# Performance work log

Hardware: AMD Instinct MI355X
Metric: run time of the kernel (lower is better)

Reference implementation:

```python
import jax, jax.numpy as jnp
import numpy as np

N = 100000        # nodes (== node_num)
E = 3200000       # edges
C = 8             # hidden (sparse=False branch)
HEADS = 2
GROUPS = 8
LAYERS = 3
FEAT = 16
EMB = 8
NCLS = 2


def glin(x, W, b):
    # PyG grouped Linear: x [..., C], W [G, C//G, C//G], b [C]
    G, cin, cout = W.shape
    xg = x.reshape(*x.shape[:-1], G, cin)
    out = jnp.einsum('...gi,gio->...go', xg, W)
    return out.reshape(*x.shape[:-1], G * cout) + b


def gcn_norm(edge_index, num_nodes):
    # symmetric GCN normalization with added self-loops, unit edge weights
    loop = jnp.arange(num_nodes, dtype=edge_index.dtype)
    src = jnp.concatenate([edge_index[0], loop])
    dst = jnp.concatenate([edge_index[1], loop])
    w = jnp.ones(src.shape[0], dtype=jnp.float32)
    deg = jax.ops.segment_sum(w, dst, num_segments=num_nodes)
    dinv = jnp.where(deg > 0, jax.lax.rsqrt(deg), 0.0)
    return src, dst, dinv[src] * dinv[dst]


def dna_conv(x_all, src, dst, norm, Wq, bq, Wk, bk, Wv, bv):
    # PyG DNAConv (eval mode): target's latest history entry attends over the
    # source neighbor's full history. x_all: [N, L, C].
    n, L, c = x_all.shape
    d = c // HEADS
    # q/k/v linears are per-entry -> compute per node, gather per edge (same math)
    q = glin(x_all[:, -1], Wq, bq).reshape(n, HEADS, d)    # [N,H,d]
    k = glin(x_all, Wk, bk).reshape(n, L, HEADS, d)        # [N,L,H,d]
    v = glin(x_all, Wv, bv).reshape(n, L, HEADS, d)
    qe = q[dst]                                            # [E',H,d]
    score = jnp.einsum('ehd,elhd->ehl', qe, k[src]) * (1.0 / np.sqrt(d))
    attn = jax.nn.softmax(score, axis=-1)                  # softmax over history L
    out = jnp.einsum('ehl,elhd->ehd', attn, v[src]).reshape(-1, c)
    out = out * norm[:, None]
    return jax.ops.segment_sum(out, dst, num_segments=n)   # aggr='add' at target


def setup_inputs():
    ks = jax.random.split(jax.random.key(0), 16)
    s = 0.5
    return {
        'x': jax.random.normal(ks[0], (N, FEAT), dtype=jnp.float32),
        'node_index': jnp.arange(N),
        'node_one_hot': jnp.zeros((N,), dtype=jnp.int32),
        'edge_index': jax.random.randint(ks[1], (2, E), 0, N),
        'edge_weight': jax.random.uniform(ks[2], (E,), dtype=jnp.float32),
        'emb_table': jax.random.normal(ks[3], (N, EMB), dtype=jnp.float32) * 0.1,
        'W1': jax.random.normal(ks[4], (EMB + FEAT, C), dtype=jnp.float32) * 0.2,
        'b1': jnp.zeros((C,), dtype=jnp.float32),
        'Wq': jax.random.normal(ks[5], (LAYERS, GROUPS, C // GROUPS, C // GROUPS), dtype=jnp.float32) * s,
        'bq': jnp.zeros((LAYERS, C), dtype=jnp.float32),
        'Wk': jax.random.normal(ks[6], (LAYERS, GROUPS, C // GROUPS, C // GROUPS), dtype=jnp.float32) * s,
        'bk': jnp.zeros((LAYERS, C), dtype=jnp.float32),
        'Wv': jax.random.normal(ks[7], (LAYERS, GROUPS, C // GROUPS, C // GROUPS), dtype=jnp.float32) * s,
        'bv': jnp.zeros((LAYERS, C), dtype=jnp.float32),
        'W2': jax.random.normal(ks[8], (C, NCLS), dtype=jnp.float32) * 0.3,
        'b2': jnp.zeros((NCLS,), dtype=jnp.float32),
    }


def reference(x, node_index, node_one_hot, edge_index, edge_weight,
              emb_table, W1, b1, Wq, bq, Wk, bk, Wv, bv, W2, b2):
    # node_one_hot / edge_weight are unpacked but unused in the original forward
    h = jnp.concatenate([emb_table[node_index], x], axis=1)   # [N, EMB+FEAT]
    h = jax.nn.relu(h @ W1 + b1)                              # [N, C]
    x_all = h[:, None, :]                                     # history [N, 1, C]
    src, dst, norm = gcn_norm(edge_index, x.shape[0])
    for i in range(LAYERS):
        h = jax.nn.relu(dna_conv(x_all, src, dst, norm,
                                 Wq[i], bq[i], Wk[i], bk[i], Wv[i], bv[i]))
        x_all = jnp.concatenate([x_all, h[:, None, :]], axis=1)
    logits = x_all[:, -1] @ W2 + b2
    return jax.nn.log_softmax(logits, axis=-1)
```

## Files before the change

kernel.cpp:

```cpp
#include <hip/hip_runtime.h>
#include <math.h>


#define SBB   8
#define SBN   256
#define CH    4096
#define CAP   9216

typedef _Float16 half8 __attribute__((ext_vector_type(8)));
typedef int int4v __attribute__((ext_vector_type(4)));

__global__ void __launch_bounds__(256) phaseAC(const int* __restrict__ eidx,
                                               int* __restrict__ gcnt,
                                               int* __restrict__ ebuf,
                                               int E, int NS) {
    __shared__ int sorted_[CH];
    __shared__ unsigned short karr[CH];
    __shared__ int cntS[512];
    __shared__ int lofs[512];
    __shared__ int wbase[512];
    __shared__ int sA[512], sB[512];
    int t = threadIdx.x, b = blockIdx.x;
    int base = b * CH;
    int nEdge = E - base; if (nEdge > CH) nEdge = CH;

    for (int i = t; i < 512; i += 256) cntS[i] = 0;
    __syncthreads();

    int w[16]; short kk[16];
#pragma unroll
    for (int it = 0; it < 4; it++) {
        int e0 = base + (it * 256 + t) * 4;
        if (e0 + 3 < E) {
            int4v s4 = __builtin_nontemporal_load((const int4v*)(eidx + e0));
            int4v d4 = __builtin_nontemporal_load((const int4v*)(eidx + E + e0));
#pragma unroll
            for (int j = 0; j < 4; j++) {
                int idx = it * 4 + j;
                w[idx] = s4[j] | ((d4[j] & (SBN - 1)) << 17);
                kk[idx] = (short)(d4[j] >> SBB);
                atomicAdd(&cntS[kk[idx]], 1);
            }
        } else {
#pragma unroll
            for (int j = 0; j < 4; j++) {
                int e = e0 + j, idx = it * 4 + j;
                if (e < E) {
                    int s = eidx[e], d = eidx[E + e];
                    w[idx] = s | ((d & (SBN - 1)) << 17);
                    kk[idx] = (short)(d >> SBB);
                    atomicAdd(&cntS[kk[idx]], 1);
                } else { w[idx] = 0; kk[idx] = 511; }
            }
        }
    }
    __syncthreads();
    sA[t] = cntS[t]; sA[t + 256] = cntS[t + 256];
    __syncthreads();
    int* sp = sA; int* dp = sB;
    for (int o = 1; o < 512; o <<= 1) {
#pragma unroll
        for (int h = 0; h < 2; h++) {
            int i = t + h * 256;
            int v = sp[i];
            if (i >= o) v += sp[i - o];
            dp[i] = v;
        }
        __syncthreads();
        int* tmp = sp; sp = dp; dp = tmp;
    }
    for (int i = t; i < 512; i += 256) {
        int excl = sp[i] - cntS[i];
        lofs[i] = excl;
        if (i < NS && cntS[i] > 0) {
            int g = atomicAdd(&gcnt[i], cntS[i]);
            wbase[i] = i * CAP + g - excl;
        }
    }
    __syncthreads();
#pragma unroll
    for (int idx = 0; idx < 16; idx++) {
        if (kk[idx] != 511) {
            int p = atomicAdd(&lofs[kk[idx]], 1);
            sorted_[p] = w[idx];
            karr[p] = (unsigned short)kk[idx];
        }
    }
    __syncthreads();
    for (int i = t; i < nEdge; i += 256)
        ebuf[wbase[karr[i]] + i] = sorted_[i];
}

__global__ void super_csr(int* __restrict__ ebuf, const int* __restrict__ gcnt,
                          unsigned int* __restrict__ off, char* __restrict__ A,
                          char* __restrict__ U, int NS, int n) {
    __shared__ int seg[CAP];
    __shared__ int cnt[SBN];
    __shared__ int fillp[SBN];
    __shared__ int sd[256];
    int t = threadIdx.x, k = blockIdx.x;
    cnt[t] = 0;
    int start = k * CAP;
    int len = gcnt[k];
    __syncthreads();
    for (int i = t; i < len; i += 256) {
        int w = __builtin_nontemporal_load(&ebuf[start + i]);
        seg[i] = w;
        atomicAdd(&cnt[w >> 17], 1);
    }
    __syncthreads();
    int v = cnt[t];
    sd[t] = v; __syncthreads();
    for (int o = 1; o < 256; o <<= 1) {
        int u = 0; if (t >= o) u = sd[t - o];
        __syncthreads(); sd[t] += u; __syncthreads();
    }
    int excl = sd[t] - v;
    fillp[t] = excl;
    int d = (k << SBB) + t;
    if (d < n) {
        off[d] = (unsigned int)(start + excl) | ((unsigned int)v << 22);
        float dvv = rsqrtf((float)(v + 1));
        *(float*)(A + (size_t)d * 32 + 16) = dvv;
        *(float*)(U + (size_t)d * 64 + 48) = dvv;
    }
    __syncthreads();
    for (int i = t; i < len; i += 256) {
        int w = seg[i];
        int pos = atomicAdd(&fillp[w >> 17], 1);
        ebuf[start + pos] = w & 131071;
    }
}

__global__ void node_init(const float* __restrict__ x, const int* __restrict__ nidx,
                          const float* __restrict__ emb, const float* __restrict__ W1,
                          const float* __restrict__ b1, char* __restrict__ A,
                          char* __restrict__ U, int n) {
    int i = blockIdx.x * blockDim.x + threadIdx.x;
    if (i >= n) return;
    float in[24];
    int ni = nidx[i];
    const float4* ep = (const float4*)(emb + (size_t)ni * 8);
    float4 e0 = ep[0], e1 = ep[1];
    in[0] = e0.x; in[1] = e0.y; in[2] = e0.z; in[3] = e0.w;
    in[4] = e1.x; in[5] = e1.y; in[6] = e1.z; in[7] = e1.w;
    const float4* xp = (const float4*)(x + (size_t)i * 16);
#pragma unroll
    for (int t = 0; t < 4; t++) {
        float4 v = xp[t];
        in[8 + 4 * t + 0] = v.x; in[8 + 4 * t + 1] = v.y;
        in[8 + 4 * t + 2] = v.z; in[8 + 4 * t + 3] = v.w;
    }
    float acc[8];
#pragma unroll
    for (int j = 0; j < 8; j++) acc[j] = b1[j];
#pragma unroll
    for (int t = 0; t < 24; t++) {
        float xv = in[t];
#pragma unroll
        for (int j = 0; j < 8; j++) acc[j] = fmaf(xv, W1[t * 8 + j], acc[j]);
    }
    half8 h;
#pragma unroll
    for (int j = 0; j < 8; j++) h[j] = (_Float16)fmaxf(acc[j], 0.0f);
    *(half8*)(A + (size_t)i * 32) = h;
    *(half8*)(U + (size_t)i * 64) = h;
}

template <int Li>
__device__ __forceinline__ void attn_out(const float* xs, const float* qv,
                                         const float* __restrict__ wk, const float* __restrict__ bk,
                                         const float* __restrict__ wv, const float* __restrict__ bv,
                                         float* out) {
    float score[2][Li];
#pragma unroll
    for (int l = 0; l < Li; l++) {
#pragma unroll
        for (int h = 0; h < 2; h++) {
            float sc = 0.f;
#pragma unroll
            for (int dd = 0; dd < 4; dd++) {
                int c = h * 4 + dd;
                sc = fmaf(qv[c], fmaf(xs[l * 8 + c], wk[c], bk[c]), sc);
            }
            score[h][l] = 0.5f * sc;
        }
    }
    float attn[2][Li];
#pragma unroll
    for (int h = 0; h < 2; h++) {
        float m = score[h][0];
#pragma unroll
        for (int l = 1; l < Li; l++) m = fmaxf(m, score[h][l]);
        float ssum = 0.f;
#pragma unroll
        for (int l = 0; l < Li; l++) { attn[h][l] = __expf(score[h][l] - m); ssum += attn[h][l]; }
        float inv = 1.0f / ssum;
#pragma unroll
        for (int l = 0; l < Li; l++) attn[h][l] *= inv;
    }
#pragma unroll
    for (int c = 0; c < 8; c++) {
        int h = c >> 2;
        float o = 0.f;
#pragma unroll
        for (int l = 0; l < Li; l++) o = fmaf(attn[h][l], fmaf(xs[l * 8 + c], wv[c], bv[c]), o);
        out[c] = o;
    }
}

template <int Li, bool LAST>
__global__ void agg_layer(const int* __restrict__ ssrc, const unsigned int* __restrict__ off,
                          const char* __restrict__ A, char* __restrict__ U,
                          const float* __restrict__ wq, const float* __restrict__ bq,
                          const float* __restrict__ wk, const float* __restrict__ bk,
                          const float* __restrict__ wv, const float* __restrict__ bv,
                          const float* __restrict__ W2, const float* __restrict__ b2,
                          float* __restrict__ out, int n) {
    int tid = blockIdx.x * blockDim.x + threadIdx.x;
    int d = tid >> 3, t = tid & 7;
    if (d >= n) return;
    unsigned int ow = off[d];
    int lo = (int)(ow & 0x3FFFFFu), cnt = (int)(ow >> 22);

    half8 qh;
    if (Li == 1) qh = *(const half8*)(A + (size_t)d * 32);
    else if (Li == 2) qh = *(const half8*)(U + (size_t)d * 64 + 16);
    else qh = *(const half8*)(U + (size_t)d * 64 + 32);
    float qv[8];
#pragma unroll
    for (int c = 0; c < 8; c++) qv[c] = fmaf((float)qh[c], wq[c], bq[c]);

    float acc[8];
#pragma unroll
    for (int c = 0; c < 8; c++) acc[c] = 0.f;

    int total = cnt + 1;
    int g = (total + 7) >> 3;
    int j0 = t * g;
    int j1 = j0 + g; if (j1 > total) j1 = total;

    for (int j = j0; j < j1; j += 4) {
        int m = j1 - j; if (m > 4) m = 4;
        int sidx[4];
#pragma unroll
        for (int u = 0; u < 4; u++) {
            int idx = j + u;
            sidx[u] = (u < m) ? ((idx == 0) ? d : ssrc[lo + idx - 1]) : d;
        }
        half8 r[4][Li]; float nsv[4];
#pragma unroll
        for (int u = 0; u < 4; u++) {
            if (u < m) {
                if (Li == 1) {
                    const char* p = A + (size_t)sidx[u] * 32;
                    r[u][0] = *(const half8*)p;
                    nsv[u] = *(const float*)(p + 16);
                } else {
                    const char* p = U + (size_t)sidx[u] * 64;
#pragma unroll
                    for (int l = 0; l < Li; l++) r[u][l] = *(const half8*)(p + l * 16);
                    nsv[u] = *(const float*)(p + 48);
                }
            }
        }
#pragma unroll
        for (int u = 0; u < 4; u++) {
            if (u < m) {
                float xs[8 * Li];
#pragma unroll
                for (int l = 0; l < Li; l++)
#pragma unroll
                    for (int c = 0; c < 8; c++) xs[l * 8 + c] = (float)r[u][l][c];
                float o[8];
                attn_out<Li>(xs, qv, wk, bk, wv, bv, o);
#pragma unroll
                for (int c = 0; c < 8; c++) acc[c] = fmaf(o[c], nsv[u], acc[c]);
            }
        }
    }
#pragma unroll
    for (int m2 = 1; m2 < 8; m2 <<= 1) {
#pragma unroll
        for (int c = 0; c < 8; c++) acc[c] += __shfl_xor(acc[c], m2);
    }
    float nd = (Li == 1) ? *(const float*)(A + (size_t)d * 32 + 16)
                         : *(const float*)(U + (size_t)d * 64 + 48);
    if (!LAST) {
        float h = fmaxf(acc[t] * nd, 0.f);
        *(_Float16*)(U + (size_t)d * 64 + Li * 16 + 2 * t) = (_Float16)h;
    } else if (t == 0) {
        float z0 = b2[0], z1 = b2[1];
#pragma unroll
        for (int c = 0; c < 8; c++) {
            float h = fmaxf(acc[c] * nd, 0.f);
            z0 = fmaf(h, W2[c * 2 + 0], z0);
            z1 = fmaf(h, W2[c * 2 + 1], z1);
        }
        float m2 = fmaxf(z0, z1);
        float lse = m2 + logf(__expf(z0 - m2) + __expf(z1 - m2));
        ((float2*)out)[d] = make_float2(z0 - lse, z1 - lse);
    }
}

extern "C" void kernel_launch(void* const* d_in, const int* in_sizes, int n_in,
                              void* d_out, int out_size, void* d_ws, size_t ws_size,
                              hipStream_t stream) {
    const float* x    = (const float*)d_in[0];
    const int*   nidx = (const int*)d_in[1];
    const int*   eidx = (const int*)d_in[3];
    const float* emb  = (const float*)d_in[5];
    const float* W1   = (const float*)d_in[6];
    const float* b1   = (const float*)d_in[7];
    const float* Wq   = (const float*)d_in[8];
    const float* bq   = (const float*)d_in[9];
    const float* Wk   = (const float*)d_in[10];
    const float* bk   = (const float*)d_in[11];
    const float* Wv   = (const float*)d_in[12];
    const float* bv   = (const float*)d_in[13];
    const float* W2   = (const float*)d_in[14];
    const float* b2   = (const float*)d_in[15];
    float* out = (float*)d_out;

    const int n = in_sizes[0] / 16;
    const int E = in_sizes[3] / 2;
    const int NS = (n + SBN - 1) / SBN;
    const int NBLK = (E + CH - 1) / CH;

    char* wsp = (char*)d_ws;
    char*  A     = wsp;                      wsp += (size_t)n * 32;
    char*  U     = wsp;                      wsp += (size_t)n * 64;
    int*   ebuf  = (int*)wsp;                wsp += (size_t)NS * CAP * 4;
    unsigned int* off = (unsigned int*)wsp;  wsp += (size_t)n * 4;
    int*   gcnt  = (int*)wsp;                wsp += (size_t)NS * 4;

    dim3 blk(256);
    dim3 gn((n + 255) / 256);
    dim3 ga(((size_t)n * 8 + 255) / 256);

    (void)hipMemsetAsync(gcnt, 0, (size_t)NS * 4, stream);
    phaseAC<<<NBLK, blk, 0, stream>>>(eidx, gcnt, ebuf, E, NS);
    super_csr<<<NS, blk, 0, stream>>>(ebuf, gcnt, off, A, U, NS, n);
    node_init<<<gn, blk, 0, stream>>>(x, nidx, emb, W1, b1, A, U, n);

    agg_layer<1, false><<<ga, blk, 0, stream>>>(ebuf, off, A, U,
        Wq, bq, Wk, bk, Wv, bv, W2, b2, out, n);
    agg_layer<2, false><<<ga, blk, 0, stream>>>(ebuf, off, A, U,
        Wq + 8, bq + 8, Wk + 8, bk + 8, Wv + 8, bv + 8, W2, b2, out, n);
    agg_layer<3, true><<<ga, blk, 0, stream>>>(ebuf, off, A, U,
        Wq + 16, bq + 16, Wk + 16, bk + 16, Wv + 16, bv + 16, W2, b2, out, n);
}
```

Baseline: 276.8 us.

## Factor V linear out of edge loop and skip softmax for single history

Uses linearity to pull the diagonal value projection (wv, bv) out of the per-edge sum: edges now accumulate a norm-weighted attention mix of the raw history plus the sum of norms, and wv/bv are applied once per node. The key scale and the 1/sqrt(d) factor are folded into the query once per node. With a single history entry the softmax is identically one, so layer 1 reduces to a plain weighted sum, and its gather batch grows from 4 to 8. This cuts per-edge arithmetic, relying on the grouped weights being diagonal (C/G = 1) and on bk being constant across history entries so it cancels in the softmax.

```diff
diff --git a/kernel.cpp b/kernel.cpp
--- a/kernel.cpp
+++ b/kernel.cpp
@@ -167,48 +167,6 @@
     *(half8*)(U + (size_t)i * 64) = h;
 }
 
-template <int Li>
-__device__ __forceinline__ void attn_out(const float* xs, const float* qv,
-                                         const float* __restrict__ wk, const float* __restrict__ bk,
-                                         const float* __restrict__ wv, const float* __restrict__ bv,
-                                         float* out) {
-    float score[2][Li];
-#pragma unroll
-    for (int l = 0; l < Li; l++) {
-#pragma unroll
-        for (int h = 0; h < 2; h++) {
-            float sc = 0.f;
-#pragma unroll
-            for (int dd = 0; dd < 4; dd++) {
-                int c = h * 4 + dd;
-                sc = fmaf(qv[c], fmaf(xs[l * 8 + c], wk[c], bk[c]), sc);
-            }
-            score[h][l] = 0.5f * sc;
-        }
-    }
-    float attn[2][Li];
-#pragma unroll
-    for (int h = 0; h < 2; h++) {
-        float m = score[h][0];
-#pragma unroll
-        for (int l = 1; l < Li; l++) m = fmaxf(m, score[h][l]);
-        float ssum = 0.f;
-#pragma unroll
-        for (int l = 0; l < Li; l++) { attn[h][l] = __expf(score[h][l] - m); ssum += attn[h][l]; }
-        float inv = 1.0f / ssum;
-#pragma unroll
-        for (int l = 0; l < Li; l++) attn[h][l] *= inv;
-    }
-#pragma unroll
-    for (int c = 0; c < 8; c++) {
-        int h = c >> 2;
-        float o = 0.f;
-#pragma unroll
-        for (int l = 0; l < Li; l++) o = fmaf(attn[h][l], fmaf(xs[l * 8 + c], wv[c], bv[c]), o);
-        out[c] = o;
-    }
-}
-
 template <int Li, bool LAST>
 __global__ void agg_layer(const int* __restrict__ ssrc, const unsigned int* __restrict__ off,
                           const char* __restrict__ A, char* __restrict__ U,
@@ -217,40 +175,44 @@
                           const float* __restrict__ wv, const float* __restrict__ bv,
                           const float* __restrict__ W2, const float* __restrict__ b2,
                           float* __restrict__ out, int n) {
+    constexpr int B = (Li == 1) ? 8 : 4;
     int tid = blockIdx.x * blockDim.x + threadIdx.x;
     int d = tid >> 3, t = tid & 7;
     if (d >= n) return;
     unsigned int ow = off[d];
     int lo = (int)(ow & 0x3FFFFFu), cnt = (int)(ow >> 22);
 
-    half8 qh;
-    if (Li == 1) qh = *(const half8*)(A + (size_t)d * 32);
-    else if (Li == 2) qh = *(const half8*)(U + (size_t)d * 64 + 16);
-    else qh = *(const half8*)(U + (size_t)d * 64 + 32);
-    float qv[8];
-#pragma unroll
-    for (int c = 0; c < 8; c++) qv[c] = fmaf((float)qh[c], wq[c], bq[c]);
-
-    float acc[8];
-#pragma unroll
-    for (int c = 0; c < 8; c++) acc[c] = 0.f;
+    float qk[8];
+    if (Li >= 2) {
+        half8 qh = (Li == 2) ? *(const half8*)(U + (size_t)d * 64 + 16)
+                             : *(const half8*)(U + (size_t)d * 64 + 32);
+#pragma unroll
+        for (int c = 0; c < 8; c++) {
+            float qv = fmaf((float)qh[c], wq[c], bq[c]);
+            qk[c] = 0.5f * wk[c] * qv;
+        }
+    }
+
+    float T[8]; float SN = 0.f;
+#pragma unroll
+    for (int c = 0; c < 8; c++) T[c] = 0.f;
 
     int total = cnt + 1;
     int g = (total + 7) >> 3;
     int j0 = t * g;
     int j1 = j0 + g; if (j1 > total) j1 = total;
 
-    for (int j = j0; j < j1; j += 4) {
-        int m = j1 - j; if (m > 4) m = 4;
-        int sidx[4];
-#pragma unroll
-        for (int u = 0; u < 4; u++) {
+    for (int j = j0; j < j1; j += B) {
+        int m = j1 - j; if (m > B) m = B;
+        int sidx[B];
+#pragma unroll
+        for (int u = 0; u < B; u++) {
             int idx = j + u;
             sidx[u] = (u < m) ? ((idx == 0) ? d : ssrc[lo + idx - 1]) : d;
         }
-        half8 r[4][Li]; float nsv[4];
-#pragma unroll
-        for (int u = 0; u < 4; u++) {
+        half8 r[B][Li]; float nsv[B];
+#pragma unroll
+        for (int u = 0; u < B; u++) {
             if (u < m) {
                 if (Li == 1) {
                     const char* p = A + (size_t)sidx[u] * 32;
@@ -265,35 +227,75 @@
             }
         }
 #pragma unroll
-        for (int u = 0; u < 4; u++) {
+        for (int u = 0; u < B; u++) {
             if (u < m) {
                 float xs[8 * Li];
 #pragma unroll
                 for (int l = 0; l < Li; l++)
 #pragma unroll
                     for (int c = 0; c < 8; c++) xs[l * 8 + c] = (float)r[u][l][c];
-                float o[8];
-                attn_out<Li>(xs, qv, wk, bk, wv, bv, o);
-#pragma unroll
-                for (int c = 0; c < 8; c++) acc[c] = fmaf(o[c], nsv[u], acc[c]);
+                float ns = nsv[u];
+                if (Li == 1) {
+#pragma unroll
+                    for (int c = 0; c < 8; c++) T[c] = fmaf(ns, xs[c], T[c]);
+                    SN += ns;
+                } else {
+                    float score[2][Li];
+#pragma unroll
+                    for (int l = 0; l < Li; l++) {
+#pragma unroll
+                        for (int h = 0; h < 2; h++) {
+                            float sc = 0.f;
+#pragma unroll
+                            for (int dd = 0; dd < 4; dd++) {
+                                int c = h * 4 + dd;
+                                sc = fmaf(qk[c], xs[l * 8 + c], sc);
+                            }
+                            score[h][l] = sc;
+                        }
+                    }
+                    float e[2][Li], nsh[2];
+#pragma unroll
+                    for (int h = 0; h < 2; h++) {
+                        float mx = score[h][0];
+#pragma unroll
+                        for (int l = 1; l < Li; l++) mx = fmaxf(mx, score[h][l]);
+                        float ssum = 0.f;
+#pragma unroll
+                        for (int l = 0; l < Li; l++) { e[h][l] = __expf(score[h][l] - mx); ssum += e[h][l]; }
+                        nsh[h] = ns / ssum;
+                    }
+#pragma unroll
+                    for (int c = 0; c < 8; c++) {
+                        int h = c >> 2;
+                        float P = 0.f;
+#pragma unroll
+                        for (int l = 0; l < Li; l++) P = fmaf(e[h][l], xs[l * 8 + c], P);
+                        T[c] = fmaf(nsh[h], P, T[c]);
+                    }
+                    SN += ns;
+                }
             }
         }
     }
 #pragma unroll
     for (int m2 = 1; m2 < 8; m2 <<= 1) {
 #pragma unroll
-        for (int c = 0; c < 8; c++) acc[c] += __shfl_xor(acc[c], m2);
+        for (int c = 0; c < 8; c++) T[c] += __shfl_xor(T[c], m2);
+        SN += __shfl_xor(SN, m2);
     }
     float nd = (Li == 1) ? *(const float*)(A + (size_t)d * 32 + 16)
                          : *(const float*)(U + (size_t)d * 64 + 48);
     if (!LAST) {
-        float h = fmaxf(acc[t] * nd, 0.f);
+        float acc = fmaf(wv[t], T[t], bv[t] * SN);
+        float h = fmaxf(acc * nd, 0.f);
         *(_Float16*)(U + (size_t)d * 64 + Li * 16 + 2 * t) = (_Float16)h;
     } else if (t == 0) {
         float z0 = b2[0], z1 = b2[1];
 #pragma unroll
         for (int c = 0; c < 8; c++) {
-            float h = fmaxf(acc[c] * nd, 0.f);
+            float acc = fmaf(wv[c], T[c], bv[c] * SN);
+            float h = fmaxf(acc * nd, 0.f);
             z0 = fmaf(h, W2[c * 2 + 0], z0);
             z1 = fmaf(h, W2[c * 2 + 1], z1);
         }
```

Measured after the change: 275.6 us. Within noise of the previous version (-0.4%).
